# Performance work log

Measured on AMD Instinct MI355X. Metric: run time of the kernel, lower is better.

The kernel has to match this reference:

```python
import jax, jax.numpy as jnp
import numpy as np

IN_C, OUT_C, K, UP, C_DIM = 128, 64, 3, 2, 512
CLAMP = 256.0
ACT_GAIN = np.sqrt(2.0)  # lrelu def_gain


def _upfirdn_up2(x, f2):
    """upfirdn2d with up=2, padding=(3,2,3,2), gain=up^2 for a 4-tap filter.

    Padding values come from conv2d_resample: p = k//2 = 1, fw = 4, up = 2 =>
    px0 = p + (fw+up-1)//2 = 3, px1 = p + (fw-up)//2 = 2.
    """
    N, C, H, W = x.shape
    px0, px1 = 3, 2
    # zero-insert upsample (interior padding) fused with edge padding;
    # trailing zero of the up-sampled signal folded into the high pad.
    x = jax.lax.pad(x, jnp.asarray(0, x.dtype),
                    ((0, 0, 0), (0, 0, 0),
                     (px0, px1 + (UP - 1), UP - 1),
                     (px0, px1 + (UP - 1), UP - 1)))
    k = (f2 * (UP * UP)).astype(x.dtype)[None, None]   # [1,1,4,4], symmetric -> flip is a no-op
    k = jnp.tile(k, (C, 1, 1, 1))                       # depthwise FIR
    return jax.lax.conv_general_dilated(
        x, k, window_strides=(1, 1), padding='VALID',
        feature_group_count=C, dimension_numbers=('NCHW', 'OIHW', 'NCHW'))


def setup_inputs() -> dict:
    key = jax.random.key(0)
    ks = jax.random.split(key, 4)
    return {
        "x": jax.random.normal(ks[0], (8, IN_C, 128, 128), jnp.float32),
        "c": jax.random.normal(ks[1], (8, C_DIM), jnp.float32),
        "weight": jax.random.normal(ks[2], (OUT_C, IN_C, K, K), jnp.float32),
        "bias": jnp.zeros((OUT_C,), jnp.float32),
        "w_affine": jax.random.normal(ks[3], (IN_C, C_DIM), jnp.float32),
        "b_affine": jnp.zeros((IN_C,), jnp.float32),
    }


def reference(x, c, weight, bias, w_affine, b_affine):
    # setup_filter: normalize separable FIR taps
    f1 = jnp.array([1.0, 3.0, 3.0, 1.0], jnp.float32)
    f1 = f1 / jnp.sum(f1)
    f2 = jnp.outer(f1, f1)

    # hyper modulation: x *= 1 + tanh(affine(c))
    y = c @ (w_affine * (1.0 / np.sqrt(C_DIM))).T + b_affine   # FullyConnectedLayer, linear
    x = x * (1.0 + jnp.tanh(y))[:, :, None, None]

    # conv2d_resample(up=2, padding=k//2, flip_weight=False)
    w = weight * (1.0 / np.sqrt(IN_C * K * K))                  # weight_gain
    x = _upfirdn_up2(x, f2)                                      # [N,C,2H+2,2W+2]
    w = w[:, :, ::-1, ::-1]                                      # flip_weight=False => true convolution
    x = jax.lax.conv_general_dilated(
        x, w.astype(x.dtype), window_strides=(1, 1), padding='VALID',
        dimension_numbers=('NCHW', 'OIHW', 'NCHW'))              # [N,OUT_C,2H,2W]

    # bias_act: lrelu(x+b)*sqrt(2), clamp at +-256 (gain=1)
    x = jax.nn.leaky_relu(x + bias[None, :, None, None], 0.2) * ACT_GAIN
    return jnp.clip(x, -CLAMP, CLAMP)
```

## Files before the change

kernel.cpp:

```cpp
#include <hip/hip_runtime.h>
#include <math.h>

#define IN_C   128
#define OUT_C  64
#define CDIM   512
#define HW     128
#define PHW    130
#define OHW    256
#define NB     8

typedef __attribute__((ext_vector_type(8))) short short8;
typedef __attribute__((ext_vector_type(4))) float f32x4;

__device__ inline unsigned short f2bf(float f) {
    unsigned int u = __float_as_uint(f);
    unsigned int r = (u + 0x7fffu + ((u >> 16) & 1u)) >> 16;
    return (unsigned short)r;
}

__device__ inline float postact(float v) {
    v = v > 0.f ? v : 0.2f * v;
    v *= 1.4142135623730951f;
    return fminf(fmaxf(v, -256.f), 256.f);
}

__device__ __forceinline__ void gload16(const void* g, void* l) {
    __builtin_amdgcn_global_load_lds(
        (const __attribute__((address_space(1))) unsigned int*)g,
        (__attribute__((address_space(3))) unsigned int*)l, 16, 0, 0);
}

__global__ __launch_bounds__(256) void prep_kernel(
    const float* __restrict__ w, unsigned short* __restrict__ wb2,
    unsigned short* __restrict__ xg,
    const float* __restrict__ c, const float* __restrict__ wa,
    const float* __restrict__ ba, float* __restrict__ gain) {
    int blk = blockIdx.x;
    if (blk < 1152) {
        int idx  = blk * 256 + threadIdx.x;
        int e    = idx & 7;
        int lane = (idx >> 3) & 63;
        int pr   = (idx >> 9) & 31;
        int kt   = idx >> 14;
        int hh = pr >> 4, kcb = (pr >> 3) & 1, wM = (pr >> 2) & 1, fi = pr & 3;
        int m   = (wM * 8 + hh * 4 + fi) * 16 + (lane & 15);
        int ic  = (kt & 1) * 64 + kcb * 32 + (lane >> 4) * 8 + e;
        int tap = kt >> 1;
        int ky = tap / 3, kx = tap % 3;
        int oc = m >> 2, ph = m & 3;
        int py = ph >> 1, px = ph & 1;
        int sy = 2 * ky + (py == 0 ? 1 : 0);
        int sx = 2 * kx + (px == 0 ? 1 : 0);
        const float k1[4] = {0.25f, 0.75f, 0.75f, 0.25f};
        float sum = 0.f;
        #pragma unroll
        for (int by = 0; by < 3; ++by) {
            int ay = sy - by;
            if (ay < 0 || ay > 3) continue;
            #pragma unroll
            for (int bx = 0; bx < 3; ++bx) {
                int ax = sx - bx;
                if (ax < 0 || ax > 3) continue;
                sum += w[((oc * IN_C + ic) * 3 + (2 - by)) * 3 + (2 - bx)] * k1[ay] * k1[ax];
            }
        }
        wb2[idx] = f2bf(sum * 0.029462782549439483f);
    } else if (blk < 1410) {
        int id = (blk - 1152) * 256 + threadIdx.x;
        int cc = id & 15;
        int t  = id >> 4;
        int p  = t % 516;
        int n  = t / 516;
        int Y, X;
        if (p < 130)      { Y = 0;   X = p; }
        else if (p < 260) { Y = 129; X = p - 130; }
        else              { int q = p - 260; Y = 1 + (q >> 1); X = (q & 1) * 129; }
        uint4 z = make_uint4(0, 0, 0, 0);
        *reinterpret_cast<uint4*>(xg + (((size_t)(n * PHW) + Y) * PHW + X) * 128 + cc * 8) = z;
    } else {
        int wave = (blk - 1410) * 4 + (threadIdx.x >> 6);
        int lane = threadIdx.x & 63;
        int n  = wave >> 7;
        int ic = wave & 127;
        const float* cp = c + n * CDIM;
        const float* wp = wa + ic * CDIM;
        float s = 0.f;
        #pragma unroll
        for (int k = 0; k < CDIM / 64; ++k) s += cp[lane + 64 * k] * wp[lane + 64 * k];
        #pragma unroll
        for (int off = 32; off > 0; off >>= 1) s += __shfl_down(s, off);
        if (lane == 0) {
            float y = s * 0.04419417382415922f + ba[ic];
            gain[n * IN_C + ic] = 1.0f + tanhf(y);
        }
    }
}

__global__ __launch_bounds__(256) void xprep_kernel(const float* __restrict__ x,
                                                    const float* __restrict__ gain,
                                                    unsigned short* __restrict__ xg) {
    int n = blockIdx.x >> 7;
    int y = blockIdx.x & 127;
    __shared__ unsigned short lds[128][130];
    int tid = threadIdx.x;
    for (int i = tid; i < 128 * 128; i += 256) {
        int ic = i >> 7, pix = i & 127;
        float v = x[(((n * IN_C + ic) * HW) + y) * HW + pix] * gain[n * IN_C + ic];
        lds[pix][ic] = f2bf(v);
    }
    __syncthreads();
    unsigned int* dst = (unsigned int*)(xg + (((size_t)(n * PHW) + y + 1) * PHW + 1) * 128);
    for (int i = tid; i < 8192; i += 256) {
        int pix = i >> 6, d = i & 63;
        int j = d >> 2, ww = d & 3;
        int js = j ^ ((pix + 1) & 7);
        dst[pix * 64 + js * 4 + ww] = *reinterpret_cast<const unsigned int*>(&lds[pix][d * 2]);
    }
}

#define MM(ACC, AF, BF) ACC = __builtin_amdgcn_mfma_f32_16x16x32_bf16(AF, BF, ACC, 0, 0, 0)

__global__ __launch_bounds__(512, 4) void conv_mfma11(
    const unsigned short* __restrict__ xg,
    const unsigned short* __restrict__ wb2,
    const float* __restrict__ bias,
    float* __restrict__ out) {
    __shared__ __align__(16) char haloB[46080];

    const int bid = blockIdx.x;
    const int wg  = ((bid & 7) << 7) + (bid >> 3);
    const int n     = wg >> 7;
    const int patch = wg & 127;
    const int Y0 = (patch >> 3) * 8;
    const int X0 = (patch & 7) * 16;
    const int tid  = threadIdx.x;
    const int lane = tid & 63;
    const int wid  = tid >> 6;
    const int q  = wid & 3;
    const int wN = wid >> 2;
    const int l16 = lane & 15;
    const int lhi = lane >> 4;
    const int pbase = wN * 4;

    const char* xgb = (const char*)xg + (size_t)n * PHW * PHW * 256;

    #pragma unroll 1
    for (int i = 0; i < 6; ++i) {
        int cc = i * 512 + tid;
        if (cc < 2880) {
            int r = cc / 288;
            int t2 = cc - r * 288;
            gload16(xgb + ((size_t)(Y0 + r) * PHW + X0) * 256 + t2 * 16,
                    haloB + (i * 512 + wid * 64) * 16);
        }
    }

    const char* abase = (const char*)wb2 + ((q >> 1) << 14) + ((q & 1) << 12) + (lane << 4);

    f32x4 acc[4][4];
    #pragma unroll
    for (int f = 0; f < 4; ++f)
        #pragma unroll
        for (int b = 0; b < 4; ++b) acc[f][b] = (f32x4)0.f;

    __syncthreads();

    short8 Aa[4], Ab[4], Bf[4];

    auto loadA = [&](short8 (&A)[4], int t, int kc) {
        const char* ak = abase + t * 32768 + kc * 8192;
        #pragma unroll
        for (int f = 0; f < 4; ++f)
            A[f] = *reinterpret_cast<const short8*>(ak + (f << 10));
    };
    auto loadB = [&](short8 (&B)[4], int rowb, int off) {
        #pragma unroll
        for (int b = 0; b < 4; ++b)
            B[b] = *reinterpret_cast<const short8*>(haloB + ((rowb + b * 18) << 8) + off);
    };
    auto cluster = [&](short8 (&A)[4], short8 (&B)[4]) {
        __builtin_amdgcn_s_setprio(1);
        #pragma unroll
        for (int f = 0; f < 4; ++f)
            #pragma unroll
            for (int b = 0; b < 4; ++b) MM(acc[f][b], A[f], B[b]);
        __builtin_amdgcn_s_setprio(0);
    };

    loadA(Aa, 0, 0);

    #pragma unroll 1
    for (int t = 0; t < 18; ++t) {
        const int tap = t >> 1;
        const int h   = t & 1;
        const int ky  = tap / 3;
        const int kx  = tap - ky * 3;
        const int C   = l16 + kx;
        const int bswz = (C & 7) << 4;
        const int rowb = (pbase + ky) * 18 + C;

        loadA(Ab, t, 1);
        loadB(Bf, rowb, ((h << 7) + (lhi << 4)) ^ bswz);
        __builtin_amdgcn_sched_barrier(0);
        cluster(Aa, Bf);

        if (t + 1 < 18) loadA(Aa, t + 1, 0);
        loadB(Bf, rowb, ((h << 7) + 64 + (lhi << 4)) ^ bswz);
        __builtin_amdgcn_sched_barrier(0);
        cluster(Ab, Bf);
    }

    #pragma unroll
    for (int f = 0; f < 4; ++f) {
        const int oc = (q & 1) * 32 + (q >> 1) * 16 + f * 4 + lhi;
        const float bi = bias[oc];
        #pragma unroll
        for (int b = 0; b < 4; ++b) {
            const int ypix = Y0 + pbase + b;
            const int xpix = X0 + l16;
            float* o0 = out + (((size_t)(n * OUT_C + oc) * OHW) + 2 * ypix) * OHW + 2 * xpix;
            float2 v0 = make_float2(postact(acc[f][b][0] + bi), postact(acc[f][b][1] + bi));
            float2 v1 = make_float2(postact(acc[f][b][2] + bi), postact(acc[f][b][3] + bi));
            *reinterpret_cast<float2*>(o0) = v0;
            *reinterpret_cast<float2*>(o0 + OHW) = v1;
        }
    }
}

__global__ void gain_kernel(const float* __restrict__ c,
                            const float* __restrict__ w_affine,
                            const float* __restrict__ b_affine,
                            float* __restrict__ gain) {
    int wave = (blockIdx.x * blockDim.x + threadIdx.x) >> 6;
    int lane = threadIdx.x & 63;
    if (wave >= NB * IN_C) return;
    int n  = wave >> 7;
    int ic = wave & 127;
    const float* cp = c + n * CDIM;
    const float* wp = w_affine + ic * CDIM;
    float s = 0.f;
    #pragma unroll
    for (int k = 0; k < CDIM / 64; ++k) s += cp[lane + 64 * k] * wp[lane + 64 * k];
    #pragma unroll
    for (int off = 32; off > 0; off >>= 1) s += __shfl_down(s, off);
    if (lane == 0) {
        float y = s * 0.04419417382415922f + b_affine[ic];
        gain[n * IN_C + ic] = 1.0f + tanhf(y);
    }
}

__global__ void wprep_kernel(const float* __restrict__ w, float* __restrict__ wp) {
    int idx = blockIdx.x * blockDim.x + threadIdx.x;
    if (idx >= IN_C * 9 * 4 * OUT_C) return;
    int oc = idx & 63;
    int t  = idx >> 6;
    int ph = t & 3;  t >>= 2;
    int kx = t % 3;  t /= 3;
    int ky = t % 3;  t /= 3;
    int ic = t;
    int py = ph >> 1, px = ph & 1;
    int sy = 2 * ky + (py == 0 ? 1 : 0);
    int sx = 2 * kx + (px == 0 ? 1 : 0);
    const float k1[4] = {0.25f, 0.75f, 0.75f, 0.25f};
    float sum = 0.f;
    #pragma unroll
    for (int by = 0; by < 3; ++by) {
        int ay = sy - by;
        if (ay < 0 || ay > 3) continue;
        #pragma unroll
        for (int bx = 0; bx < 3; ++bx) {
            int ax = sx - bx;
            if (ax < 0 || ax > 3) continue;
            sum += w[((oc * IN_C + ic) * 3 + (2 - by)) * 3 + (2 - bx)] * k1[ay] * k1[ax];
        }
    }
    wp[idx] = sum * 0.029462782549439483f;
}

__global__ __launch_bounds__(256) void conv_main(
    const float* __restrict__ x, const float* __restrict__ gain,
    const float* __restrict__ wp, const float* __restrict__ bias,
    float* __restrict__ out) {
    const int n    = blockIdx.z >> 3;
    const int occ  = (blockIdx.z & 7) * 8;
    const int tx0  = blockIdx.x * 16;
    const int ty0  = blockIdx.y * 16;
    const int tid  = threadIdx.x;
    const int lx   = tid & 15;
    const int ly   = tid >> 4;
    __shared__ float xsf[8][18][18];
    float acc[4][8];
    #pragma unroll
    for (int p = 0; p < 4; ++p)
        #pragma unroll
        for (int o = 0; o < 8; ++o) acc[p][o] = 0.f;
    for (int ic0 = 0; ic0 < IN_C; ic0 += 8) {
        __syncthreads();
        for (int i = tid; i < 8 * 324; i += 256) {
            int icb = i / 324;
            int rem = i - icb * 324;
            int yy  = rem / 18;
            int xx  = rem - yy * 18;
            int gy  = ty0 + yy - 1;
            int gx  = tx0 + xx - 1;
            int ic  = ic0 + icb;
            float v = 0.f;
            if (gy >= 0 && gy < HW && gx >= 0 && gx < HW)
                v = x[((n * IN_C + ic) * HW + gy) * HW + gx] * gain[n * IN_C + ic];
            xsf[icb][yy][xx] = v;
        }
        __syncthreads();
        for (int icb = 0; icb < 8; ++icb) {
            const int ic = ic0 + icb;
            const float* wpp = wp + ic * (9 * 4 * OUT_C) + occ;
            #pragma unroll
            for (int ky = 0; ky < 3; ++ky)
                #pragma unroll
                for (int kx = 0; kx < 3; ++kx) {
                    float tv = xsf[icb][ly + ky][lx + kx];
                    const float* w9 = wpp + (ky * 3 + kx) * (4 * OUT_C);
                    #pragma unroll
                    for (int p = 0; p < 4; ++p)
                        #pragma unroll
                        for (int o = 0; o < 8; ++o)
                            acc[p][o] = fmaf(tv, w9[p * OUT_C + o], acc[p][o]);
                }
        }
    }
    const int ybase = 2 * (ty0 + ly);
    const int xbase = 2 * (tx0 + lx);
    #pragma unroll
    for (int o = 0; o < 8; ++o) {
        float b = bias[occ + o];
        #pragma unroll
        for (int py = 0; py < 2; ++py) {
            float2 v;
            v.x = postact(acc[py * 2 + 0][o] + b);
            v.y = postact(acc[py * 2 + 1][o] + b);
            *reinterpret_cast<float2*>(
                &out[((size_t)(n * OUT_C + occ + o) * OHW + (ybase + py)) * OHW + xbase]) = v;
        }
    }
}

extern "C" void kernel_launch(void* const* d_in, const int* in_sizes, int n_in,
                              void* d_out, int out_size, void* d_ws, size_t ws_size,
                              hipStream_t stream) {
    const float* x        = (const float*)d_in[0];
    const float* c        = (const float*)d_in[1];
    const float* weight   = (const float*)d_in[2];
    const float* bias     = (const float*)d_in[3];
    const float* w_affine = (const float*)d_in[4];
    const float* b_affine = (const float*)d_in[5];
    float* out = (float*)d_out;

    float* gain = (float*)d_ws;

    const size_t NEED = 1048576 + (size_t)NB * PHW * PHW * IN_C * 2;
    if (ws_size >= NEED) {
        unsigned short* wb2 = (unsigned short*)((char*)d_ws + 8192);
        unsigned short* xg  = (unsigned short*)((char*)d_ws + 1048576);
        prep_kernel<<<dim3(1666), dim3(256), 0, stream>>>(weight, wb2, xg, c, w_affine, b_affine, gain);
        xprep_kernel<<<dim3(NB * HW), dim3(256), 0, stream>>>(x, gain, xg);
        conv_mfma11<<<dim3(1024), dim3(512), 0, stream>>>(xg, wb2, bias, out);
    } else {
        float* wp = (float*)((char*)d_ws + 8192);
        gain_kernel<<<dim3((NB * IN_C * 64) / 256), dim3(256), 0, stream>>>(c, w_affine, b_affine, gain);
        wprep_kernel<<<dim3((IN_C * 9 * 4 * OUT_C + 255) / 256), dim3(256), 0, stream>>>(weight, wp);
        conv_main<<<dim3(HW / 16, HW / 16, NB * 8), dim3(256), 0, stream>>>(x, gain, wp, bias, out);
    }
}
```

Baseline: 100.3 us.

## Switch padded activation layout to channel-block-major rows for unswizzled LDS halo

Changes the bf16 padded input layout from pixel-major with 128 contiguous channels and an XOR swizzle to a per-row layout of 16 channel blocks, each holding 130 pixels. xprep writes the new layout, the halo loader gathers it in that order, and the conv inner loop addresses B fragments by channel block with constant offsets instead of swizzled ones. The loop is restructured to go over 9 taps with four MFMA clusters each. The aim is cheaper LDS addressing and conflict-free B reads without the swizzle. The risk is that global halo loads become more fragmented (18-pixel runs per channel block) and that the new LDS strides may cause bank conflicts.

```diff
diff --git a/kernel.cpp b/kernel.cpp
--- a/kernel.cpp
+++ b/kernel.cpp
@@ -29,6 +29,7 @@
         (const __attribute__((address_space(1))) unsigned int*)g,
         (__attribute__((address_space(3))) unsigned int*)l, 16, 0, 0);
 }
+
 
 __global__ __launch_bounds__(256) void prep_kernel(
     const float* __restrict__ w, unsigned short* __restrict__ wb2,
@@ -76,7 +77,8 @@
         else if (p < 260) { Y = 129; X = p - 130; }
         else              { int q = p - 260; Y = 1 + (q >> 1); X = (q & 1) * 129; }
         uint4 z = make_uint4(0, 0, 0, 0);
-        *reinterpret_cast<uint4*>(xg + (((size_t)(n * PHW) + Y) * PHW + X) * 128 + cc * 8) = z;
+        *reinterpret_cast<uint4*>(
+            xg + ((((size_t)(n * PHW) + Y) * 16 + cc) * 130 + X) * 8) = z;
     } else {
         int wave = (blk - 1410) * 4 + (threadIdx.x >> 6);
         int lane = threadIdx.x & 63;
@@ -101,7 +103,7 @@
                                                     unsigned short* __restrict__ xg) {
     int n = blockIdx.x >> 7;
     int y = blockIdx.x & 127;
-    __shared__ unsigned short lds[128][130];
+    __shared__ unsigned short lds[128][132];
     int tid = threadIdx.x;
     for (int i = tid; i < 128 * 128; i += 256) {
         int ic = i >> 7, pix = i & 127;
@@ -109,18 +111,20 @@
         lds[pix][ic] = f2bf(v);
     }
     __syncthreads();
-    unsigned int* dst = (unsigned int*)(xg + (((size_t)(n * PHW) + y + 1) * PHW + 1) * 128);
+    unsigned int* dst = (unsigned int*)xg + ((size_t)(n * PHW) + y + 1) * (16 * 130 * 4);
     for (int i = tid; i < 8192; i += 256) {
-        int pix = i >> 6, d = i & 63;
-        int j = d >> 2, ww = d & 3;
-        int js = j ^ ((pix + 1) & 7);
-        dst[pix * 64 + js * 4 + ww] = *reinterpret_cast<const unsigned int*>(&lds[pix][d * 2]);
+        int j   = i >> 9;
+        int rem = i & 511;
+        int pix = rem >> 2;
+        int w   = i & 3;
+        dst[(j * 130 + pix + 1) * 4 + w] =
+            *reinterpret_cast<const unsigned int*>(&lds[pix][(j * 4 + w) * 2]);
     }
 }
 
 #define MM(ACC, AF, BF) ACC = __builtin_amdgcn_mfma_f32_16x16x32_bf16(AF, BF, ACC, 0, 0, 0)
 
-__global__ __launch_bounds__(512, 4) void conv_mfma11(
+__global__ __launch_bounds__(512, 4) void conv_mfma12(
     const unsigned short* __restrict__ xg,
     const unsigned short* __restrict__ wb2,
     const float* __restrict__ bias,
@@ -142,15 +146,17 @@
     const int lhi = lane >> 4;
     const int pbase = wN * 4;
 
-    const char* xgb = (const char*)xg + (size_t)n * PHW * PHW * 256;
+    const char* xgb = (const char*)xg + (size_t)n * PHW * 33280;
 
     #pragma unroll 1
     for (int i = 0; i < 6; ++i) {
         int cc = i * 512 + tid;
         if (cc < 2880) {
-            int r = cc / 288;
+            int r  = cc / 288;
             int t2 = cc - r * 288;
-            gload16(xgb + ((size_t)(Y0 + r) * PHW + X0) * 256 + t2 * 16,
+            int j  = t2 / 18;
+            int px = t2 - j * 18;
+            gload16(xgb + (((size_t)(Y0 + r) * 16 + j) * 130 + X0 + px) * 16,
                     haloB + (i * 512 + wid * 64) * 16);
         }
     }
@@ -167,16 +173,15 @@
 
     short8 Aa[4], Ab[4], Bf[4];
 
-    auto loadA = [&](short8 (&A)[4], int t, int kc) {
-        const char* ak = abase + t * 32768 + kc * 8192;
+    auto loadA = [&](short8 (&A)[4], int off) {
         #pragma unroll
         for (int f = 0; f < 4; ++f)
-            A[f] = *reinterpret_cast<const short8*>(ak + (f << 10));
+            A[f] = *reinterpret_cast<const short8*>(abase + off + (f << 10));
     };
-    auto loadB = [&](short8 (&B)[4], int rowb, int off) {
+    auto ldB = [&](short8 (&B)[4], const char* bB, int joff) {
         #pragma unroll
         for (int b = 0; b < 4; ++b)
-            B[b] = *reinterpret_cast<const short8*>(haloB + ((rowb + b * 18) << 8) + off);
+            B[b] = *reinterpret_cast<const short8*>(bB + joff + b * 4608);
     };
     auto cluster = [&](short8 (&A)[4], short8 (&B)[4]) {
         __builtin_amdgcn_s_setprio(1);
@@ -187,25 +192,32 @@
         __builtin_amdgcn_s_setprio(0);
     };
 
-    loadA(Aa, 0, 0);
+    loadA(Aa, 0);
 
     #pragma unroll 1
-    for (int t = 0; t < 18; ++t) {
-        const int tap = t >> 1;
-        const int h   = t & 1;
-        const int ky  = tap / 3;
-        const int kx  = tap - ky * 3;
-        const int C   = l16 + kx;
-        const int bswz = (C & 7) << 4;
-        const int rowb = (pbase + ky) * 18 + C;
-
-        loadA(Ab, t, 1);
-        loadB(Bf, rowb, ((h << 7) + (lhi << 4)) ^ bswz);
+    for (int tap = 0; tap < 9; ++tap) {
+        const int ky = tap / 3;
+        const int kx = tap - ky * 3;
+        const char* bB = haloB + ((pbase + ky) * 4608 + lhi * 288 + (l16 + kx) * 16);
+        const int aoff = tap * 65536;
+
+        loadA(Ab, aoff + 8192);
+        ldB(Bf, bB, 0);
         __builtin_amdgcn_sched_barrier(0);
         cluster(Aa, Bf);
 
-        if (t + 1 < 18) loadA(Aa, t + 1, 0);
-        loadB(Bf, rowb, ((h << 7) + 64 + (lhi << 4)) ^ bswz);
+        loadA(Aa, aoff + 32768);
+        ldB(Bf, bB, 4 * 288);
+        __builtin_amdgcn_sched_barrier(0);
+        cluster(Ab, Bf);
+
+        loadA(Ab, aoff + 40960);
+        ldB(Bf, bB, 8 * 288);
+        __builtin_amdgcn_sched_barrier(0);
+        cluster(Aa, Bf);
+
+        if (tap < 8) loadA(Aa, aoff + 65536);
+        ldB(Bf, bB, 12 * 288);
         __builtin_amdgcn_sched_barrier(0);
         cluster(Ab, Bf);
     }
@@ -362,7 +374,7 @@
         unsigned short* xg  = (unsigned short*)((char*)d_ws + 1048576);
         prep_kernel<<<dim3(1666), dim3(256), 0, stream>>>(weight, wb2, xg, c, w_affine, b_affine, gain);
         xprep_kernel<<<dim3(NB * HW), dim3(256), 0, stream>>>(x, gain, xg);
-        conv_mfma11<<<dim3(1024), dim3(512), 0, stream>>>(xg, wb2, bias, out);
+        conv_mfma12<<<dim3(1024), dim3(512), 0, stream>>>(xg, wb2, bias, out);
     } else {
         float* wp = (float*)((char*)d_ws + 8192);
         gain_kernel<<<dim3((NB * IN_C * 64) / 256), dim3(256), 0, stream>>>(c, w_affine, b_affine, gain);
```

Measured after the change: 175.0 us. 1.74x slower.

## Stage conv weight tiles through double-buffered LDS instead of per-wave global loads

Applied to the files above, without the earlier changes.

The conv kernel previously loaded weight fragments straight from global memory into registers in every wave. Now each workgroup cooperatively copies each 16KB weight slice into one of two LDS buffers with global_load_lds, and waves read their fragments from LDS. The prep kernel's weight layout is reordered to match. This cuts redundant global/L2 weight traffic across waves, but adds a full vmcnt wait plus a workgroup barrier twice per tap, and raises LDS use to about 77KB, which may lower occupancy.

```diff
diff --git a/kernel.cpp b/kernel.cpp
--- a/kernel.cpp
+++ b/kernel.cpp
@@ -40,11 +40,12 @@
         int idx  = blk * 256 + threadIdx.x;
         int e    = idx & 7;
         int lane = (idx >> 3) & 63;
-        int pr   = (idx >> 9) & 31;
+        int f    = (idx >> 9) & 3;
+        int q    = (idx >> 11) & 3;
+        int kc   = (idx >> 13) & 1;
         int kt   = idx >> 14;
-        int hh = pr >> 4, kcb = (pr >> 3) & 1, wM = (pr >> 2) & 1, fi = pr & 3;
-        int m   = (wM * 8 + hh * 4 + fi) * 16 + (lane & 15);
-        int ic  = (kt & 1) * 64 + kcb * 32 + (lane >> 4) * 8 + e;
+        int m   = (((q & 1) * 8) + ((q >> 1) * 4) + f) * 16 + (lane & 15);
+        int ic  = (kt & 1) * 64 + kc * 32 + (lane >> 4) * 8 + e;
         int tap = kt >> 1;
         int ky = tap / 3, kx = tap % 3;
         int oc = m >> 2, ph = m & 3;
@@ -74,7 +75,7 @@
         int Y, X;
         if (p < 130)      { Y = 0;   X = p; }
         else if (p < 260) { Y = 129; X = p - 130; }
-        else              { int q = p - 260; Y = 1 + (q >> 1); X = (q & 1) * 129; }
+        else              { int qq = p - 260; Y = 1 + (qq >> 1); X = (qq & 1) * 129; }
         uint4 z = make_uint4(0, 0, 0, 0);
         *reinterpret_cast<uint4*>(xg + (((size_t)(n * PHW) + Y) * PHW + X) * 128 + cc * 8) = z;
     } else {
@@ -120,12 +121,12 @@
 
 #define MM(ACC, AF, BF) ACC = __builtin_amdgcn_mfma_f32_16x16x32_bf16(AF, BF, ACC, 0, 0, 0)
 
-__global__ __launch_bounds__(512, 4) void conv_mfma11(
+__global__ __launch_bounds__(512, 4) void conv_mfma13(
     const unsigned short* __restrict__ xg,
     const unsigned short* __restrict__ wb2,
     const float* __restrict__ bias,
     float* __restrict__ out) {
-    __shared__ __align__(16) char haloB[46080];
+    __shared__ __align__(16) char smem[78848];
 
     const int bid = blockIdx.x;
     const int wg  = ((bid & 7) << 7) + (bid >> 3);
@@ -142,20 +143,31 @@
     const int lhi = lane >> 4;
     const int pbase = wN * 4;
 
-    const char* xgb = (const char*)xg + (size_t)n * PHW * PHW * 256;
+    char* haloB = smem;
+    char* abuf0 = smem + 46080;
+    char* abuf1 = smem + 46080 + 16384;
+
+    const char* xgb  = (const char*)xg + (size_t)n * PHW * PHW * 256;
+    const char* wb2b = (const char*)wb2;
 
     #pragma unroll 1
     for (int i = 0; i < 6; ++i) {
         int cc = i * 512 + tid;
         if (cc < 2880) {
-            int r = cc / 288;
+            int r  = cc / 288;
             int t2 = cc - r * 288;
             gload16(xgb + ((size_t)(Y0 + r) * PHW + X0) * 256 + t2 * 16,
                     haloB + (i * 512 + wid * 64) * 16);
         }
     }
 
-    const char* abase = (const char*)wb2 + ((q >> 1) << 14) + ((q & 1) << 12) + (lane << 4);
+    auto stageA = [&](int s, char* buf) {
+        const char* src = wb2b + s * 16384;
+        gload16(src + tid * 16,        buf + (wid * 64) * 16);
+        gload16(src + 8192 + tid * 16, buf + 8192 + (wid * 64) * 16);
+    };
+
+    const int aoff = q * 4096 + lane * 16;
 
     f32x4 acc[4][4];
     #pragma unroll
@@ -163,31 +175,29 @@
         #pragma unroll
         for (int b = 0; b < 4; ++b) acc[f][b] = (f32x4)0.f;
 
+    stageA(0, abuf0);
     __syncthreads();
 
-    short8 Aa[4], Ab[4], Bf[4];
-
-    auto loadA = [&](short8 (&A)[4], int t, int kc) {
-        const char* ak = abase + t * 32768 + kc * 8192;
+    short8 Areg[4], Bf[4];
+
+    auto ldA = [&](const char* buf) {
         #pragma unroll
         for (int f = 0; f < 4; ++f)
-            A[f] = *reinterpret_cast<const short8*>(ak + (f << 10));
+            Areg[f] = *reinterpret_cast<const short8*>(buf + aoff + (f << 10));
     };
-    auto loadB = [&](short8 (&B)[4], int rowb, int off) {
+    auto ldB = [&](int rowb, int off) {
         #pragma unroll
         for (int b = 0; b < 4; ++b)
-            B[b] = *reinterpret_cast<const short8*>(haloB + ((rowb + b * 18) << 8) + off);
+            Bf[b] = *reinterpret_cast<const short8*>(haloB + ((rowb + b * 18) << 8) + off);
     };
-    auto cluster = [&](short8 (&A)[4], short8 (&B)[4]) {
+    auto cluster = [&]() {
         __builtin_amdgcn_s_setprio(1);
         #pragma unroll
         for (int f = 0; f < 4; ++f)
             #pragma unroll
-            for (int b = 0; b < 4; ++b) MM(acc[f][b], A[f], B[b]);
+            for (int b = 0; b < 4; ++b) MM(acc[f][b], Areg[f], Bf[b]);
         __builtin_amdgcn_s_setprio(0);
     };
-
-    loadA(Aa, 0, 0);
 
     #pragma unroll 1
     for (int t = 0; t < 18; ++t) {
@@ -198,16 +208,25 @@
         const int C   = l16 + kx;
         const int bswz = (C & 7) << 4;
         const int rowb = (pbase + ky) * 18 + C;
-
-        loadA(Ab, t, 1);
-        loadB(Bf, rowb, ((h << 7) + (lhi << 4)) ^ bswz);
+        const int s0 = t * 2;
+
+        stageA(s0 + 1, abuf1);
+        ldA(abuf0);
+        ldB(rowb, ((h << 7) + (lhi << 4)) ^ bswz);
         __builtin_amdgcn_sched_barrier(0);
-        cluster(Aa, Bf);
-
-        if (t + 1 < 18) loadA(Aa, t + 1, 0);
-        loadB(Bf, rowb, ((h << 7) + 64 + (lhi << 4)) ^ bswz);
+        cluster();
         __builtin_amdgcn_sched_barrier(0);
-        cluster(Ab, Bf);
+        asm volatile("s_waitcnt vmcnt(0)" ::: "memory");
+        __builtin_amdgcn_s_barrier();
+
+        if (t < 17) stageA(s0 + 2, abuf0);
+        ldA(abuf1);
+        ldB(rowb, ((h << 7) + 64 + (lhi << 4)) ^ bswz);
+        __builtin_amdgcn_sched_barrier(0);
+        cluster();
+        __builtin_amdgcn_sched_barrier(0);
+        asm volatile("s_waitcnt vmcnt(0)" ::: "memory");
+        __builtin_amdgcn_s_barrier();
     }
 
     #pragma unroll
@@ -362,7 +381,7 @@
         unsigned short* xg  = (unsigned short*)((char*)d_ws + 1048576);
         prep_kernel<<<dim3(1666), dim3(256), 0, stream>>>(weight, wb2, xg, c, w_affine, b_affine, gain);
         xprep_kernel<<<dim3(NB * HW), dim3(256), 0, stream>>>(x, gain, xg);
-        conv_mfma11<<<dim3(1024), dim3(512), 0, stream>>>(xg, wb2, bias, out);
+        conv_mfma13<<<dim3(1024), dim3(512), 0, stream>>>(xg, wb2, bias, out);
     } else {
         float* wp = (float*)((char*)d_ws + 8192);
         gain_kernel<<<dim3((NB * IN_C * 64) / 256), dim3(256), 0, stream>>>(c, w_affine, b_affine, gain);
```

Result: slower. 103.6 us (+3.2%).

## Switch conv main loop to 32x32x16 bf16 MFMA with new weight layout

Applied to the files above, without the earlier changes.

Replaces the 16x16x32 MFMA tiling with 32x32x16 bf16 MFMA instructions. Each wave now computes 2x2 tiles of 32x32 instead of 4x4 tiles of 16x16. The weight prepack layout in prep_kernel and the halo B-fragment addressing are reworked to match the 32-wide operand layout, and the epilogue is remapped to the new accumulator lane layout. The aim is fewer MFMA issues and fewer LDS/global fragment loads per FLOP. In exchange the accumulators are larger 16-float vectors, which may raise register pressure, and the LDS access pattern changes.

```diff
diff --git a/kernel.cpp b/kernel.cpp
--- a/kernel.cpp
+++ b/kernel.cpp
@@ -11,6 +11,7 @@
 
 typedef __attribute__((ext_vector_type(8))) short short8;
 typedef __attribute__((ext_vector_type(4))) float f32x4;
+typedef __attribute__((ext_vector_type(16))) float f32x16;
 
 __device__ inline unsigned short f2bf(float f) {
     unsigned int u = __float_as_uint(f);
@@ -40,12 +41,13 @@
         int idx  = blk * 256 + threadIdx.x;
         int e    = idx & 7;
         int lane = (idx >> 3) & 63;
-        int pr   = (idx >> 9) & 31;
-        int kt   = idx >> 14;
-        int hh = pr >> 4, kcb = (pr >> 3) & 1, wM = (pr >> 2) & 1, fi = pr & 3;
-        int m   = (wM * 8 + hh * 4 + fi) * 16 + (lane & 15);
-        int ic  = (kt & 1) * 64 + kcb * 32 + (lane >> 4) * 8 + e;
-        int tap = kt >> 1;
+        int im   = (idx >> 9) & 1;
+        int q    = (idx >> 10) & 3;
+        int s16  = idx >> 12;
+        int m  = q * 64 + im * 32 + (lane & 31);
+        int k  = s16 * 16 + ((lane >> 5) << 3) + e;
+        int tap = k >> 7;
+        int ic  = k & 127;
         int ky = tap / 3, kx = tap % 3;
         int oc = m >> 2, ph = m & 3;
         int py = ph >> 1, px = ph & 1;
@@ -74,7 +76,7 @@
         int Y, X;
         if (p < 130)      { Y = 0;   X = p; }
         else if (p < 260) { Y = 129; X = p - 130; }
-        else              { int q = p - 260; Y = 1 + (q >> 1); X = (q & 1) * 129; }
+        else              { int qq = p - 260; Y = 1 + (qq >> 1); X = (qq & 1) * 129; }
         uint4 z = make_uint4(0, 0, 0, 0);
         *reinterpret_cast<uint4*>(xg + (((size_t)(n * PHW) + Y) * PHW + X) * 128 + cc * 8) = z;
     } else {
@@ -118,9 +120,9 @@
     }
 }
 
-#define MM(ACC, AF, BF) ACC = __builtin_amdgcn_mfma_f32_16x16x32_bf16(AF, BF, ACC, 0, 0, 0)
-
-__global__ __launch_bounds__(512, 4) void conv_mfma11(
+#define MM32(ACC, AF, BF) ACC = __builtin_amdgcn_mfma_f32_32x32x16_bf16(AF, BF, ACC, 0, 0, 0)
+
+__global__ __launch_bounds__(512, 4) void conv_mfma14(
     const unsigned short* __restrict__ xg,
     const unsigned short* __restrict__ wb2,
     const float* __restrict__ bias,
@@ -136,10 +138,11 @@
     const int tid  = threadIdx.x;
     const int lane = tid & 63;
     const int wid  = tid >> 6;
-    const int q  = wid & 3;
-    const int wN = wid >> 2;
-    const int l16 = lane & 15;
-    const int lhi = lane >> 4;
+    const int q    = wid & 3;
+    const int wN   = wid >> 2;
+    const int l16  = lane & 15;
+    const int l16b = (lane >> 4) & 1;
+    const int lhi5 = lane >> 5;
     const int pbase = wN * 4;
 
     const char* xgb = (const char*)xg + (size_t)n * PHW * PHW * 256;
@@ -148,46 +151,54 @@
     for (int i = 0; i < 6; ++i) {
         int cc = i * 512 + tid;
         if (cc < 2880) {
-            int r = cc / 288;
+            int r  = cc / 288;
             int t2 = cc - r * 288;
             gload16(xgb + ((size_t)(Y0 + r) * PHW + X0) * 256 + t2 * 16,
                     haloB + (i * 512 + wid * 64) * 16);
         }
     }
 
-    const char* abase = (const char*)wb2 + ((q >> 1) << 14) + ((q & 1) << 12) + (lane << 4);
-
-    f32x4 acc[4][4];
-    #pragma unroll
-    for (int f = 0; f < 4; ++f)
-        #pragma unroll
-        for (int b = 0; b < 4; ++b) acc[f][b] = (f32x4)0.f;
+    const char* abase = (const char*)wb2 + (q << 11) + (lane << 4);
+
+    f32x16 acc[2][2];
+    #pragma unroll
+    for (int im = 0; im < 2; ++im)
+        #pragma unroll
+        for (int jn = 0; jn < 2; ++jn) acc[im][jn] = (f32x16)0.f;
 
     __syncthreads();
 
     short8 Aa[4], Ab[4], Bf[4];
 
-    auto loadA = [&](short8 (&A)[4], int t, int kc) {
-        const char* ak = abase + t * 32768 + kc * 8192;
-        #pragma unroll
-        for (int f = 0; f < 4; ++f)
-            A[f] = *reinterpret_cast<const short8*>(ak + (f << 10));
+    auto loadA = [&](short8 (&A)[4], int hs) {
+        const char* base = abase + hs * 16384;
+        #pragma unroll
+        for (int im = 0; im < 2; ++im)
+            #pragma unroll
+            for (int ks = 0; ks < 2; ++ks)
+                A[im * 2 + ks] = *reinterpret_cast<const short8*>(base + ks * 8192 + im * 1024);
     };
-    auto loadB = [&](short8 (&B)[4], int rowb, int off) {
-        #pragma unroll
-        for (int b = 0; b < 4; ++b)
-            B[b] = *reinterpret_cast<const short8*>(haloB + ((rowb + b * 18) << 8) + off);
+    auto ldB = [&](int rowb, int jbase, int xk) {
+        #pragma unroll
+        for (int jn = 0; jn < 2; ++jn)
+            #pragma unroll
+            for (int ks = 0; ks < 2; ++ks)
+                Bf[jn * 2 + ks] = *reinterpret_cast<const short8*>(
+                    haloB + ((rowb + jn * 36) << 8) + (((jbase + ks * 2 + lhi5) ^ xk) << 4));
     };
-    auto cluster = [&](short8 (&A)[4], short8 (&B)[4]) {
+    auto cluster = [&](short8 (&A)[4]) {
         __builtin_amdgcn_s_setprio(1);
         #pragma unroll
-        for (int f = 0; f < 4; ++f)
-            #pragma unroll
-            for (int b = 0; b < 4; ++b) MM(acc[f][b], A[f], B[b]);
+        for (int im = 0; im < 2; ++im)
+            #pragma unroll
+            for (int jn = 0; jn < 2; ++jn) {
+                MM32(acc[im][jn], A[im * 2 + 0], Bf[jn * 2 + 0]);
+                MM32(acc[im][jn], A[im * 2 + 1], Bf[jn * 2 + 1]);
+            }
         __builtin_amdgcn_s_setprio(0);
     };
 
-    loadA(Aa, 0, 0);
+    loadA(Aa, 0);
 
     #pragma unroll 1
     for (int t = 0; t < 18; ++t) {
@@ -195,36 +206,40 @@
         const int h   = t & 1;
         const int ky  = tap / 3;
         const int kx  = tap - ky * 3;
-        const int C   = l16 + kx;
-        const int bswz = (C & 7) << 4;
-        const int rowb = (pbase + ky) * 18 + C;
-
-        loadA(Ab, t, 1);
-        loadB(Bf, rowb, ((h << 7) + (lhi << 4)) ^ bswz);
+        const int X   = l16 + kx;
+        const int xk  = X & 7;
+        const int rowb = (pbase + l16b + ky) * 18 + X;
+
+        loadA(Ab, 2 * t + 1);
+        ldB(rowb, h * 8, xk);
         __builtin_amdgcn_sched_barrier(0);
-        cluster(Aa, Bf);
-
-        if (t + 1 < 18) loadA(Aa, t + 1, 0);
-        loadB(Bf, rowb, ((h << 7) + 64 + (lhi << 4)) ^ bswz);
+        cluster(Aa);
+
+        if (t + 1 < 18) loadA(Aa, 2 * t + 2);
+        ldB(rowb, h * 8 + 4, xk);
         __builtin_amdgcn_sched_barrier(0);
-        cluster(Ab, Bf);
-    }
-
-    #pragma unroll
-    for (int f = 0; f < 4; ++f) {
-        const int oc = (q & 1) * 32 + (q >> 1) * 16 + f * 4 + lhi;
-        const float bi = bias[oc];
-        #pragma unroll
-        for (int b = 0; b < 4; ++b) {
-            const int ypix = Y0 + pbase + b;
+        cluster(Ab);
+    }
+
+    #pragma unroll
+    for (int im = 0; im < 2; ++im)
+        #pragma unroll
+        for (int jn = 0; jn < 2; ++jn) {
+            const int ypix = Y0 + pbase + jn * 2 + l16b;
             const int xpix = X0 + l16;
-            float* o0 = out + (((size_t)(n * OUT_C + oc) * OHW) + 2 * ypix) * OHW + 2 * xpix;
-            float2 v0 = make_float2(postact(acc[f][b][0] + bi), postact(acc[f][b][1] + bi));
-            float2 v1 = make_float2(postact(acc[f][b][2] + bi), postact(acc[f][b][3] + bi));
-            *reinterpret_cast<float2*>(o0) = v0;
-            *reinterpret_cast<float2*>(o0 + OHW) = v1;
-        }
-    }
+            #pragma unroll
+            for (int g = 0; g < 4; ++g) {
+                const int oc = q * 16 + im * 8 + 2 * g + lhi5;
+                const float bi = bias[oc];
+                float* o0 = out + (((size_t)(n * OUT_C + oc) * OHW) + 2 * ypix) * OHW + 2 * xpix;
+                float2 v0 = make_float2(postact(acc[im][jn][4 * g + 0] + bi),
+                                        postact(acc[im][jn][4 * g + 1] + bi));
+                float2 v1 = make_float2(postact(acc[im][jn][4 * g + 2] + bi),
+                                        postact(acc[im][jn][4 * g + 3] + bi));
+                *reinterpret_cast<float2*>(o0) = v0;
+                *reinterpret_cast<float2*>(o0 + OHW) = v1;
+            }
+        }
 }
 
 __global__ void gain_kernel(const float* __restrict__ c,
@@ -362,7 +377,7 @@
         unsigned short* xg  = (unsigned short*)((char*)d_ws + 1048576);
         prep_kernel<<<dim3(1666), dim3(256), 0, stream>>>(weight, wb2, xg, c, w_affine, b_affine, gain);
         xprep_kernel<<<dim3(NB * HW), dim3(256), 0, stream>>>(x, gain, xg);
-        conv_mfma11<<<dim3(1024), dim3(512), 0, stream>>>(xg, wb2, bias, out);
+        conv_mfma14<<<dim3(1024), dim3(512), 0, stream>>>(xg, wb2, bias, out);
     } else {
         float* wp = (float*)((char*)d_ws + 8192);
         gain_kernel<<<dim3((NB * IN_C * 64) / 256), dim3(256), 0, stream>>>(c, w_affine, b_affine, gain);
```

After: 116.5 us. 16.1% more time.
